# Kernel tuning notes

Hardware: AMD Instinct MI355X
Metric: run time of the kernel (lower is better)

The kernel has to match this reference:

```python
import jax, jax.numpy as jnp
import numpy as np

B, N, DIM, H, DH = 2, 1024, 1024, 8, 64
DI = H * DH  # 512
K = 4        # depthwise conv kernel
EPS = 1.1920929e-07  # float32 eps (torch RMSNorm default)


def setup_inputs() -> dict:
    key = jax.random.key(0)
    ks = jax.random.split(key, 12)
    s = lambda k, shape, sc=0.02: jax.random.normal(k, shape, jnp.float32) * sc
    return dict(
        x=jax.random.normal(ks[0], (B, N, DIM), jnp.float32),
        w_rms=jnp.ones((DIM,), jnp.float32),
        wq=s(ks[1], (DIM, DI)), wk=s(ks[2], (DIM, DI)), wv=s(ks[3], (DIM, DI)),
        wo=s(ks[4], (DI, DIM)),
        conv_q=s(ks[5], (DIM, K), 0.3), conv_k=s(ks[6], (DIM, K), 0.3), conv_v=s(ks[7], (DIM, K), 0.3),
        gamma_q=jnp.ones((H, 1, DH), jnp.float32), gamma_k=jnp.ones((H, 1, DH), jnp.float32),
        lr_w=s(ks[8], (DIM, H)), lr_b=jnp.full((H,), -4.0, jnp.float32),
        decay_w=s(ks[9], (DIM, H)), decay_b=jnp.full((H,), 4.0, jnp.float32),
        mom_w=s(ks[10], (DIM, H)), mom_b=jnp.full((H,), 2.0, jnp.float32),
    )


def rmsnorm(x, w):
    return x * jax.lax.rsqrt(jnp.mean(x * x, -1, keepdims=True) + EPS) * w


def mh_rmsnorm(x, gamma):  # x: (b, h, n, d)
    rms = jnp.sqrt(jnp.sum(x * x, -1, keepdims=True)) * (DH ** -0.5)
    return x / jnp.maximum(rms, 1e-8) * gamma


def dwconv(x, w):  # x: (b, n, dim), w: (dim, K) depthwise, padding K//2 -> length n+1
    y = jax.lax.conv_general_dilated(
        x.transpose(0, 2, 1), w[:, None, :], (1,), [(K // 2, K // 2)],
        feature_group_count=DIM, dimension_numbers=('NCW', 'OIW', 'NCW'))
    return y.transpose(0, 2, 1)


def gated_scan(a, x):  # h_t = a_t h_{t-1} + x_t, h_{-1}=0; a:(bh,t), x:(bh,t,d,d)
    def combine(c1, c2):
        a1, x1 = c1
        a2, x2 = c2
        return a1 * a2, a2 * x1 + x2
    _, h = jax.lax.associative_scan(combine, (a[..., None, None], x), axis=1)
    return h


def reference(x, w_rms, wq, wk, wv, wo, conv_q, conv_k, conv_v,
              gamma_q, gamma_k, lr_w, lr_b, decay_w, decay_b, mom_w, mom_b):
    b, n, _ = x.shape
    xa = rmsnorm(x, w_rms)
    qi, ki, vi = dwconv(xa, conv_q), dwconv(xa, conv_k), dwconv(xa, conv_v)
    split = lambda t: t.reshape(b, -1, H, DH).transpose(0, 2, 1, 3)[:, :, :n]  # (b,h,n,d)
    q = mh_rmsnorm(split(qi @ wq), gamma_q)
    k = mh_rmsnorm(split(ki @ wk), gamma_k)
    v = split(vi @ wv)
    fq = q.reshape(b * H, n, DH)
    fk = k.reshape(b * H, n, DH)
    fv = v.reshape(b * H, n, DH)
    sig = jax.nn.sigmoid
    lr = sig(xa @ lr_w + lr_b).transpose(0, 2, 1).reshape(b * H, n)
    decay = sig(xa @ decay_w + decay_b).transpose(0, 2, 1).reshape(b * H, n)
    mom = sig(xa @ mom_w + mom_b).transpose(0, 2, 1).reshape(b * H, n)
    # S_ref = S0 = 0 (fresh state) => pred = 0, delta_vec = -v
    g = jnp.einsum('bti,btj->btij', -fv, fk)          # (bh, n, d, d)
    Z = gated_scan(mom, g)                             # momentum scan
    S = gated_scan(decay, -lr[..., None, None] * Z)    # memory scan
    S_prev = jnp.concatenate([jnp.zeros_like(S[:, :1]), S[:, :-1]], axis=1)
    y = jnp.einsum('btdp,btp->btd', S_prev, fq)        # retrieval y_t = S_{t-1} psi_t
    y = y.reshape(b, H, n, DH).transpose(0, 2, 1, 3).reshape(b, n, DI)
    return y @ wo
```

## Files before the change

kernel.cpp:

```cpp
#include <hip/hip_runtime.h>
#include <math.h>

#define DEV __device__ __forceinline__

constexpr int Bb   = 2;
constexpr int Seq  = 1024;
constexpr int Dim  = 1024;
constexpr int Hh   = 8;
constexpr int Dh   = 64;
constexpr int Di   = 512;
constexpr int BN   = Bb * Seq;
constexpr int NSEQ = Bb * Hh;
constexpr int CHUNK = 32;
constexpr int CLEN  = Seq / CHUNK;
constexpr float EPSV = 1.1920929e-07f;
constexpr int NT2  = 8;
constexpr int KSPL = 8;

typedef _Float16 half8 __attribute__((ext_vector_type(8)));
typedef float    f32x4 __attribute__((ext_vector_type(4)));

DEV float bf2f(unsigned short u) {
  union { unsigned int i; float f; } x; x.i = ((unsigned int)u) << 16; return x.f;
}
DEV unsigned short f2bf(float f) {
  union { float f; unsigned int i; } x; x.f = f;
  unsigned int r = x.i + 0x7fffu + ((x.i >> 16) & 1u);
  return (unsigned short)(r >> 16);
}
DEV float ldin(const void* p, int f32, size_t i) {
  if (f32) return ((const float*)p)[i];
  return bf2f(((const unsigned short*)p)[i]);
}
DEV void ld4(const void* p, int f32, size_t i, float* dst) {
  if (f32) {
    float4 u = *(const float4*)((const float*)p + i);
    dst[0] = u.x; dst[1] = u.y; dst[2] = u.z; dst[3] = u.w;
  } else {
    ushort4 u = *(const ushort4*)((const unsigned short*)p + i);
    dst[0] = bf2f(u.x); dst[1] = bf2f(u.y); dst[2] = bf2f(u.z); dst[3] = bf2f(u.w);
  }
}
DEV int sniff_vote(const void* p, int n, int tid) {
  int j = 2 * tid, valid = 0, bad = 0;
  if (j < n) {
    valid = 1;
    float v = bf2f(((const unsigned short*)p)[j]);
    float a = fabsf(v);
    if (!(a >= 1e-12f && a <= 1e4f)) bad = 1;
  }
#pragma unroll
  for (int m = 1; m < 64; m <<= 1) { valid += __shfl_xor(valid, m); bad += __shfl_xor(bad, m); }
  return (2 * bad > valid) ? 1 : 0;
}

DEV void gld16(const _Float16* g, _Float16* l) {
  __builtin_amdgcn_global_load_lds(
      (const __attribute__((address_space(1))) void*)g,
      (__attribute__((address_space(3))) void*)l, 16, 0, 0);
}

struct InPtrs { const void* p[17]; int n[17]; };

__global__ __launch_bounds__(256) void k_prep_all(
    InPtrs ip,
    int* __restrict__ flags,
    _Float16* __restrict__ wqT, _Float16* __restrict__ wkT,
    _Float16* __restrict__ wvT, _Float16* __restrict__ woT,
    _Float16* __restrict__ WgT,
    _Float16* __restrict__ wcq, _Float16* __restrict__ wck,
    _Float16* __restrict__ wcv,
    float* __restrict__ gqf, float* __restrict__ gkf, float* __restrict__ gbf)
{
  int blk = blockIdx.x;
  int tid = threadIdx.x;
  __shared__ int sfl[8];

  if (blk < 1024) {
    int z = blk >> 8, bx = blk & 15, by = (blk >> 4) & 15;
    int idx = (z == 0) ? 2 : ((z == 1) ? 3 : ((z == 2) ? 4 : 5));
    const void* src = ip.p[idx];
    _Float16* dst   = (z == 0) ? wqT : ((z == 1) ? wkT : ((z == 2) ? wvT : woT));
    int Kd = (z < 3) ? Dim : Di;
    int Nn = (z < 3) ? Di : Dim;
    int n0 = bx * 64, k0 = by * 64;
    if (n0 >= Nn || k0 >= Kd) return;

    if (tid < 64) { int f = sniff_vote(src, ip.n[idx], tid); if (tid == 0) sfl[0] = f; }
    __syncthreads();
    int f = sfl[0];

    __shared__ float tile[64][65];
    int r = tid >> 4, c4 = (tid & 15) * 4;
#pragma unroll
    for (int rr = 0; rr < 4; ++rr) {
      int k = rr * 16 + r;
      ld4(src, f, (size_t)(k0 + k) * Nn + n0 + c4, &tile[k][c4]);
    }
    __syncthreads();
#pragma unroll
    for (int rr = 0; rr < 4; ++rr) {
      int n = rr * 16 + r;
      _Float16 o4[4];
#pragma unroll
      for (int j = 0; j < 4; ++j) o4[j] = (_Float16)tile[c4 + j][n];
      *(ushort4*)&dst[(size_t)(n0 + n) * Kd + k0 + c4] = *(ushort4*)o4;
    }
  } else if (blk < 1088) {
    int row = blk - 1024;
    if (row < 24) {
      int g = row >> 3, h = row & 7;
      int idx = (g == 0) ? 11 : ((g == 1) ? 13 : 15);
      const void* W = ip.p[idx];
      if (tid < 64) { int f = sniff_vote(W, ip.n[idx], tid); if (tid == 0) sfl[0] = f; }
      __syncthreads();
      int f = sfl[0];
#pragma unroll
      for (int it = 0; it < 4; ++it) {
        int d = it * 256 + tid;
        WgT[(size_t)row * Dim + d] = (_Float16)ldin(W, f, (size_t)d * Hh + h);
      }
    } else {
#pragma unroll
      for (int it = 0; it < 4; ++it)
        WgT[(size_t)row * Dim + it * 256 + tid] = (_Float16)0.f;
    }
  } else if (blk < 1104) {
    if (tid < 64) {
      int f6 = sniff_vote(ip.p[6], ip.n[6], tid);
      int f7 = sniff_vote(ip.p[7], ip.n[7], tid);
      int f8 = sniff_vote(ip.p[8], ip.n[8], tid);
      if (tid == 0) { sfl[0] = f6; sfl[1] = f7; sfl[2] = f8; }
    }
    __syncthreads();
    int e = (blk - 1088) * 256 + tid;
    wcq[e] = (_Float16)ldin(ip.p[6], sfl[0], e);
    wck[e] = (_Float16)ldin(ip.p[7], sfl[1], e);
    wcv[e] = (_Float16)ldin(ip.p[8], sfl[2], e);
  } else {
    __shared__ int allf[17];
    for (int ii = 0; ii < 17; ++ii) {
      if (tid < 64) {
        int f = sniff_vote(ip.p[ii], ip.n[ii], tid);
        if (tid == 0) { flags[ii] = f; allf[ii] = f; }
      }
    }
    __syncthreads();
    int f9 = allf[9], f10 = allf[10];
    for (int i = tid; i < Di; i += 256) {
      gqf[i] = ldin(ip.p[9], f9, i);
      gkf[i] = ldin(ip.p[10], f10, i);
    }
    if (tid < 24) {
      int g = tid >> 3, h = tid & 7;
      int idx = (g == 0) ? 12 : ((g == 1) ? 14 : 16);
      gbf[tid] = ldin(ip.p[idx], allf[idx], h);
    }
  }
}

__global__ __launch_bounds__(256) void k_rmsconv(
    const void* __restrict__ x, const void* __restrict__ w_rms,
    const int* __restrict__ flags,
    const _Float16* __restrict__ wcq, const _Float16* __restrict__ wck,
    const _Float16* __restrict__ wcv,
    _Float16* __restrict__ xaf,
    _Float16* __restrict__ qc, _Float16* __restrict__ kc,
    _Float16* __restrict__ vc)
{
  constexpr int NR = NT2 + 3;
  __shared__ _Float16 xas[NR][Dim];
  int tb = blockIdx.x, b = blockIdx.y;
  int t0 = tb * NT2;
  int tid = threadIdx.x, lane = tid & 63, wv = tid >> 6;
  int fx = flags[0], fw = flags[1];
  int e0 = lane * 16;

  float wr[16];
#pragma unroll
  for (int q = 0; q < 4; ++q) ld4(w_rms, fw, e0 + q * 4, &wr[q * 4]);

  for (int rr = wv; rr < NR; rr += 4) {
    int r = t0 - 2 + rr;
    float xv[16];
    bool inr = (r >= 0 && r < Seq);
    if (inr) {
      size_t rb = (size_t)(b * Seq + r) * Dim + e0;
#pragma unroll
      for (int q = 0; q < 4; ++q) ld4(x, fx, rb + q * 4, &xv[q * 4]);
    } else {
#pragma unroll
      for (int j = 0; j < 16; ++j) xv[j] = 0.f;
    }
    float ss = 0.f;
#pragma unroll
    for (int j = 0; j < 16; ++j) ss = fmaf(xv[j], xv[j], ss);
#pragma unroll
    for (int m = 1; m < 64; m <<= 1) ss += __shfl_xor(ss, m);
    float scale = rsqrtf(ss * (1.0f / Dim) + EPSV);

    _Float16 o[16];
#pragma unroll
    for (int j = 0; j < 16; ++j) o[j] = (_Float16)(xv[j] * scale * wr[j]);
    *(uint4*)&xas[rr][e0]     = *(uint4*)&o[0];
    *(uint4*)&xas[rr][e0 + 8] = *(uint4*)&o[8];
    if (inr && r >= t0 && r < t0 + NT2) {
      size_t ob = (size_t)(b * Seq + r) * Dim + e0;
      *(uint4*)&xaf[ob]     = *(uint4*)&o[0];
      *(uint4*)&xaf[ob + 8] = *(uint4*)&o[8];
    }
  }
  __syncthreads();

  int c0 = tid * 4;
  _Float16 lwq[16], lwk[16], lwv[16];
  *(uint4*)&lwq[0] = *(const uint4*)&wcq[c0 * 4];
  *(uint4*)&lwq[8] = *(const uint4*)&wcq[c0 * 4 + 8];
  *(uint4*)&lwk[0] = *(const uint4*)&wck[c0 * 4];
  *(uint4*)&lwk[8] = *(const uint4*)&wck[c0 * 4 + 8];
  *(uint4*)&lwv[0] = *(const uint4*)&wcv[c0 * 4];
  *(uint4*)&lwv[8] = *(const uint4*)&wcv[c0 * 4 + 8];

#pragma unroll
  for (int tt = 0; tt < NT2; ++tt) {
    float rv[4][4];
#pragma unroll
    for (int k = 0; k < 4; ++k) {
      _Float16 hx[4];
      *(ushort4*)hx = *(const ushort4*)&xas[tt + k][c0];
#pragma unroll
      for (int j = 0; j < 4; ++j) rv[k][j] = (float)hx[j];
    }
    _Float16 tq[4], tk[4], tv[4];
#pragma unroll
    for (int j = 0; j < 4; ++j) {
      float aq = rv[0][j] * (float)lwq[j * 4 + 0] + rv[1][j] * (float)lwq[j * 4 + 1]
               + rv[2][j] * (float)lwq[j * 4 + 2] + rv[3][j] * (float)lwq[j * 4 + 3];
      float ak = rv[0][j] * (float)lwk[j * 4 + 0] + rv[1][j] * (float)lwk[j * 4 + 1]
               + rv[2][j] * (float)lwk[j * 4 + 2] + rv[3][j] * (float)lwk[j * 4 + 3];
      float av = rv[0][j] * (float)lwv[j * 4 + 0] + rv[1][j] * (float)lwv[j * 4 + 1]
               + rv[2][j] * (float)lwv[j * 4 + 2] + rv[3][j] * (float)lwv[j * 4 + 3];
      tq[j] = (_Float16)aq; tk[j] = (_Float16)ak; tv[j] = (_Float16)av;
    }
    size_t o = ((size_t)(b * Seq + t0 + tt)) * Dim + c0;
    *(ushort4*)&qc[o] = *(ushort4*)tq;
    *(ushort4*)&kc[o] = *(ushort4*)tk;
    *(ushort4*)&vc[o] = *(ushort4*)tv;
  }
}

__global__ __launch_bounds__(256) void k_mid(
    const _Float16* __restrict__ qc, const _Float16* __restrict__ kc,
    const _Float16* __restrict__ vc,
    const _Float16* __restrict__ wqT, const _Float16* __restrict__ wkT,
    const _Float16* __restrict__ wvT,
    const _Float16* __restrict__ xaf, const _Float16* __restrict__ WgT,
    _Float16* __restrict__ qpre, _Float16* __restrict__ kpre,
    _Float16* __restrict__ vpre,
    float* __restrict__ gpart)
{
  __shared__ __align__(16) _Float16 ldsbuf[256 * 32];

  int blk = blockIdx.x;
  int tid = threadIdx.x, lane = tid & 63, wv = tid >> 6;
  int mrow = lane & 15, quad = lane >> 4;

  if (blk < 192) {
    int z = blk >> 6, rem = blk & 63;
    int by = rem >> 2, bx = rem & 3;
    const _Float16* A  = (z == 0) ? qc : ((z == 1) ? kc : vc);
    const _Float16* Bt = (z == 0) ? wqT : ((z == 1) ? wkT : wvT);
    _Float16* C        = (z == 0) ? qpre : ((z == 1) ? kpre : vpre);
    int m0 = by * 128, n0 = bx * 128;
    int wr = wv >> 1, wc = wv & 1;

    _Float16* Asl = ldsbuf;
    _Float16* Bsl = ldsbuf + 128 * 32;

    int sr = lane >> 2, sc = (lane & 3) * 8;

    f32x4 acc[4][4];
#pragma unroll
    for (int mi = 0; mi < 4; ++mi)
#pragma unroll
      for (int ni = 0; ni < 4; ++ni) acc[mi][ni] = (f32x4){0.f, 0.f, 0.f, 0.f};

    for (int kt = 0; kt < Dim; kt += 32) {
      __syncthreads();
      gld16(&A [(size_t)(m0 + wv * 32      + sr) * Dim + kt + sc], &Asl[(wv * 32     ) * 32]);
      gld16(&A [(size_t)(m0 + wv * 32 + 16 + sr) * Dim + kt + sc], &Asl[(wv * 32 + 16) * 32]);
      gld16(&Bt[(size_t)(n0 + wv * 32      + sr) * Dim + kt + sc], &Bsl[(wv * 32     ) * 32]);
      gld16(&Bt[(size_t)(n0 + wv * 32 + 16 + sr) * Dim + kt + sc], &Bsl[(wv * 32 + 16) * 32]);
      __syncthreads();

      half8 afr[4], bfr[4];
#pragma unroll
      for (int i = 0; i < 4; ++i)
        afr[i] = *(const half8*)&Asl[(wr * 64 + i * 16 + mrow) * 32 + quad * 8];
#pragma unroll
      for (int i = 0; i < 4; ++i)
        bfr[i] = *(const half8*)&Bsl[(wc * 64 + i * 16 + mrow) * 32 + quad * 8];
#pragma unroll
      for (int mi = 0; mi < 4; ++mi)
#pragma unroll
        for (int ni = 0; ni < 4; ++ni)
          acc[mi][ni] = __builtin_amdgcn_mfma_f32_16x16x32_f16(afr[mi], bfr[ni], acc[mi][ni], 0, 0, 0);
    }

#pragma unroll
    for (int mi = 0; mi < 4; ++mi) {
#pragma unroll
      for (int ni = 0; ni < 4; ++ni) {
        int col = n0 + wc * 64 + ni * 16 + mrow;
#pragma unroll
        for (int r2 = 0; r2 < 4; ++r2) {
          int row = m0 + wr * 64 + mi * 16 + quad * 4 + r2;
          C[(size_t)row * Di + col] = (_Float16)acc[mi][ni][r2];
        }
      }
    }
  } else {
    _Float16 (*As)[40] = (_Float16(*)[40])ldsbuf;
    _Float16 (*Bs)[40] = (_Float16(*)[40])(ldsbuf + 128 * 40);

    int g = blk - 192;
    int m0 = (g & 31) * 64, ks = g >> 5;
    int srow = tid >> 2, scol = (tid & 3) * 8;
    int kbase = ks * (Dim / KSPL);

    f32x4 acc[4];
#pragma unroll
    for (int mi = 0; mi < 4; ++mi) acc[mi] = (f32x4){0.f, 0.f, 0.f, 0.f};

    for (int kt = kbase; kt < kbase + Dim / KSPL; kt += 32) {
      __syncthreads();
      *(uint4*)&As[srow][scol] = *(const uint4*)&xaf[(size_t)(m0 + srow) * Dim + kt + scol];
      *(uint4*)&Bs[srow][scol] = *(const uint4*)&WgT[(size_t)srow * Dim + kt + scol];
      __syncthreads();
      half8 bfr = *(const half8*)&Bs[wv * 16 + mrow][quad * 8];
#pragma unroll
      for (int mi = 0; mi < 4; ++mi) {
        half8 afr = *(const half8*)&As[mi * 16 + mrow][quad * 8];
        acc[mi] = __builtin_amdgcn_mfma_f32_16x16x32_f16(afr, bfr, acc[mi], 0, 0, 0);
      }
    }

    int col = wv * 16 + mrow;
    if (col < 24) {
#pragma unroll
      for (int mi = 0; mi < 4; ++mi) {
#pragma unroll
        for (int r2 = 0; r2 < 4; ++r2) {
          int row = m0 + mi * 16 + quad * 4 + r2;
          gpart[((size_t)ks * BN + row) * 32 + col] = acc[mi][r2];
        }
      }
    }
  }
}

__global__ __launch_bounds__(256) void k_gemm_fin(
    const _Float16* __restrict__ A, const _Float16* __restrict__ Bt,
    void* __restrict__ C, const int* __restrict__ flags, int Nn, int Kd)
{
  __shared__ __align__(16) _Float16 lds[(128 + 64) * 32];
  _Float16* Asl = lds;
  _Float16* Bsl = lds + 128 * 32;

  int tid = threadIdx.x, lane = tid & 63, wv = tid >> 6;
  int n0 = blockIdx.x * 64, m0 = blockIdx.y * 128;
  int mrow = lane & 15, quad = lane >> 4;
  int wm = wv * 32;
  int sr = lane >> 2, sc = (lane & 3) * 8;

  f32x4 acc[2][4];
#pragma unroll
  for (int mi = 0; mi < 2; ++mi)
#pragma unroll
    for (int ni = 0; ni < 4; ++ni) acc[mi][ni] = (f32x4){0.f, 0.f, 0.f, 0.f};

  for (int kt = 0; kt < Kd; kt += 32) {
    __syncthreads();
    gld16(&A [(size_t)(m0 + wv * 32      + sr) * Kd + kt + sc], &Asl[(wv * 32     ) * 32]);
    gld16(&A [(size_t)(m0 + wv * 32 + 16 + sr) * Kd + kt + sc], &Asl[(wv * 32 + 16) * 32]);
    gld16(&Bt[(size_t)(n0 + wv * 16      + sr) * Kd + kt + sc], &Bsl[(wv * 16     ) * 32]);
    __syncthreads();

    half8 bfr[4];
#pragma unroll
    for (int ni = 0; ni < 4; ++ni)
      bfr[ni] = *(const half8*)&Bsl[(ni * 16 + mrow) * 32 + quad * 8];
#pragma unroll
    for (int mi = 0; mi < 2; ++mi) {
      half8 afr = *(const half8*)&Asl[(wm + mi * 16 + mrow) * 32 + quad * 8];
#pragma unroll
      for (int ni = 0; ni < 4; ++ni)
        acc[mi][ni] = __builtin_amdgcn_mfma_f32_16x16x32_f16(afr, bfr[ni], acc[mi][ni], 0, 0, 0);
    }
  }

  int any_bf16 = 0;
#pragma unroll
  for (int i2 = 0; i2 < 17; ++i2) any_bf16 |= (flags[i2] == 0);

#pragma unroll
  for (int mi = 0; mi < 2; ++mi) {
#pragma unroll
    for (int ni = 0; ni < 4; ++ni) {
      int col = n0 + ni * 16 + mrow;
#pragma unroll
      for (int r2 = 0; r2 < 4; ++r2) {
        int row = m0 + wm + mi * 16 + quad * 4 + r2;
        float v = acc[mi][ni][r2];
        size_t idx = (size_t)row * Nn + col;
        if (any_bf16) ((unsigned short*)C)[idx] = f2bf(v);
        else          ((float*)C)[idx] = v;
      }
    }
  }
}

DEV void load_gates(const float* __restrict__ gpart, const float* __restrict__ gbf,
                    int b, int h, int c, int tid,
                    float* gl, float* gd, float* gm)
{
  if (tid < 96) {
    int which = tid >> 5, t2 = tid & 31;
    int col = which * 8 + h;
    int row = b * Seq + c * CLEN + t2;
    float acc = gbf[col];
#pragma unroll
    for (int ks = 0; ks < KSPL; ++ks)
      acc += gpart[((size_t)ks * BN + row) * 32 + col];
    float sg = 1.f / (1.f + expf(-acc));
    if (which == 0) gl[t2] = sg; else if (which == 1) gd[t2] = sg; else gm[t2] = sg;
  }
}

__global__ __launch_bounds__(256) void k_phaseA(
    const _Float16* __restrict__ kpre, const _Float16* __restrict__ vpre,
    const float* __restrict__ gkf,
    const float* __restrict__ gpart, const float* __restrict__ gbf,
    _Float16* __restrict__ ZS_Z, _Float16* __restrict__ ZS_S,
    float* __restrict__ Mc, float* __restrict__ Dc, float* __restrict__ Wc)
{
  int c = blockIdx.x, s = blockIdx.y;
  int b = s >> 3, h = s & 7;
  int tid = threadIdx.x, lane = tid & 63, wv = tid >> 6;
  int i = tid >> 2, j0 = (tid & 3) * 16;
  __shared__ float kn[CLEN][64], vv[CLEN][64];
  __shared__ float gl[CLEN], gd[CLEN], gm[CLEN];

  {
    int t = tid >> 3, col = (tid & 7) * 8;
    size_t g = ((size_t)(b * Seq + c * CLEN + t)) * Di + h * 64 + col;
    half8 kv = *(const half8*)&kpre[g];
    half8 vvv = *(const half8*)&vpre[g];
#pragma unroll
    for (int j = 0; j < 8; ++j) { kn[t][col + j] = (float)kv[j]; vv[t][col + j] = (float)vvv[j]; }
    load_gates(gpart, gbf, b, h, c, tid, gl, gd, gm);
  }
  __syncthreads();
  {
    float gk = gkf[h * 64 + lane];
#pragma unroll
    for (int tt = 0; tt < 8; ++tt) {
      int t = wv * 8 + tt;
      float kvv = kn[t][lane];
      float ss = kvv * kvv;
#pragma unroll
      for (int m = 1; m < 64; m <<= 1) ss += __shfl_xor(ss, m);
      kn[t][lane] = kvv * (1.f / fmaxf(sqrtf(ss) * 0.125f, 1e-8f)) * gk;
    }
  }
  __syncthreads();

  float Zl[16], Sl[16];
#pragma unroll
  for (int jj = 0; jj < 16; ++jj) { Zl[jj] = 0.f; Sl[jj] = 0.f; }
  float Mcum = 1.f, Dcum = 1.f, wacc = 0.f;

  for (int t = 0; t < CLEN; ++t) {
    float l = gl[t], dd = gd[t], mm = gm[t];
    float vi = vv[t][i];
    Mcum *= mm;
#pragma unroll
    for (int jj = 0; jj < 16; ++jj) {
      Zl[jj] = fmaf(mm, Zl[jj], -vi * kn[t][j0 + jj]);
      Sl[jj] = fmaf(dd, Sl[jj], -l * Zl[jj]);
    }
    wacc = fmaf(dd, wacc, -l * Mcum);
    Dcum *= dd;
  }
  size_t base = ((size_t)(s * CHUNK + c)) * 4096 + (size_t)i * 64 + j0;
  half8 zo0, zo1, so0, so1;
#pragma unroll
  for (int jj = 0; jj < 8; ++jj) {
    zo0[jj] = (_Float16)Zl[jj];     zo1[jj] = (_Float16)Zl[jj + 8];
    so0[jj] = (_Float16)Sl[jj];     so1[jj] = (_Float16)Sl[jj + 8];
  }
  *(half8*)&ZS_Z[base] = zo0; *(half8*)&ZS_Z[base + 8] = zo1;
  *(half8*)&ZS_S[base] = so0; *(half8*)&ZS_S[base + 8] = so1;
  if (tid == 0) {
    Mc[s * CHUNK + c] = Mcum; Dc[s * CHUNK + c] = Dcum; Wc[s * CHUNK + c] = wacc;
  }
}

__global__ __launch_bounds__(256) void k_phaseB(
    _Float16* __restrict__ ZS_Z, _Float16* __restrict__ ZS_S,
    const float* __restrict__ Mc, const float* __restrict__ Dc,
    const float* __restrict__ Wc)
{
  int s = blockIdx.x;
  int e = blockIdx.y * 256 + threadIdx.x;
  float Z = 0.f, S = 0.f;
  for (int c = 0; c < CHUNK; ++c) {
    size_t base = ((size_t)(s * CHUNK + c)) * 4096 + e;
    float mc = Mc[s * CHUNK + c], dc = Dc[s * CHUNK + c], wc = Wc[s * CHUNK + c];
    float zl = (float)ZS_Z[base], sl = (float)ZS_S[base];
    ZS_Z[base] = (_Float16)Z; ZS_S[base] = (_Float16)S;
    S = fmaf(dc, S, fmaf(wc, Z, sl));
    Z = fmaf(mc, Z, zl);
  }
}

__global__ __launch_bounds__(256) void k_phaseC(
    const _Float16* __restrict__ qpre, const _Float16* __restrict__ kpre,
    const _Float16* __restrict__ vpre,
    const float* __restrict__ gqf, const float* __restrict__ gkf,
    const float* __restrict__ gpart, const float* __restrict__ gbf,
    const _Float16* __restrict__ ZS_Z, const _Float16* __restrict__ ZS_S,
    _Float16* __restrict__ yb)
{
  int c = blockIdx.x, s = blockIdx.y;
  int b = s >> 3, h = s & 7;
  int tid = threadIdx.x, lane = tid & 63, wv = tid >> 6;
  int i = tid >> 2, j0 = (tid & 3) * 16;
  __shared__ float kn[CLEN][64], vv[CLEN][64], qn[CLEN][64];
  __shared__ float gl[CLEN], gd[CLEN], gm[CLEN];

  float Zi_[16], Si_[16], Zl[16], Sl[16];
  size_t base = ((size_t)(s * CHUNK + c)) * 4096 + (size_t)i * 64 + j0;
  {
    half8 z0 = *(const half8*)&ZS_Z[base], z1 = *(const half8*)&ZS_Z[base + 8];
    half8 s0 = *(const half8*)&ZS_S[base], s1 = *(const half8*)&ZS_S[base + 8];
#pragma unroll
    for (int jj = 0; jj < 8; ++jj) {
      Zi_[jj] = (float)z0[jj]; Zi_[jj + 8] = (float)z1[jj];
      Si_[jj] = (float)s0[jj]; Si_[jj + 8] = (float)s1[jj];
      Zl[jj] = 0.f; Zl[jj + 8] = 0.f; Sl[jj] = 0.f; Sl[jj + 8] = 0.f;
    }
  }
  {
    int t = tid >> 3, col = (tid & 7) * 8;
    size_t g = ((size_t)(b * Seq + c * CLEN + t)) * Di + h * 64 + col;
    half8 kv = *(const half8*)&kpre[g];
    half8 vvv = *(const half8*)&vpre[g];
    half8 qv = *(const half8*)&qpre[g];
#pragma unroll
    for (int j = 0; j < 8; ++j) {
      kn[t][col + j] = (float)kv[j]; vv[t][col + j] = (float)vvv[j];
      qn[t][col + j] = (float)qv[j];
    }
    load_gates(gpart, gbf, b, h, c, tid, gl, gd, gm);
  }
  __syncthreads();
  {
    float gk = gkf[h * 64 + lane];
    float gq = gqf[h * 64 + lane];
#pragma unroll
    for (int tt = 0; tt < 8; ++tt) {
      int t = wv * 8 + tt;
      float kvv = kn[t][lane];
      float ssk = kvv * kvv;
      float qvv = qn[t][lane];
      float ssq = qvv * qvv;
#pragma unroll
      for (int m = 1; m < 64; m <<= 1) { ssk += __shfl_xor(ssk, m); ssq += __shfl_xor(ssq, m); }
      kn[t][lane] = kvv * (1.f / fmaxf(sqrtf(ssk) * 0.125f, 1e-8f)) * gk;
      qn[t][lane] = qvv * (1.f / fmaxf(sqrtf(ssq) * 0.125f, 1e-8f)) * gq;
    }
  }
  __syncthreads();

  float Mcum = 1.f, Dcum = 1.f, wacc = 0.f;
  float Dprev = 1.f, wprev = 0.f;

  for (int t = 0; t < CLEN; ++t) {
    float l = gl[t], dd = gd[t], mm = gm[t];

    float yp = 0.f;
#pragma unroll
    for (int jj = 0; jj < 16; ++jj) {
      float tmp = fmaf(Dprev, Si_[jj], fmaf(wprev, Zi_[jj], Sl[jj]));
      yp = fmaf(tmp, qn[t][j0 + jj], yp);
    }
    yp += __shfl_xor(yp, 1);
    yp += __shfl_xor(yp, 2);
    if ((tid & 3) == 0)
      yb[((size_t)(b * Seq + c * CLEN + t)) * Di + h * 64 + i] = (_Float16)yp;

    float vi = vv[t][i];
    Mcum *= mm;
#pragma unroll
    for (int jj = 0; jj < 16; ++jj) {
      Zl[jj] = fmaf(mm, Zl[jj], -vi * kn[t][j0 + jj]);
      Sl[jj] = fmaf(dd, Sl[jj], -l * Zl[jj]);
    }
    wacc = fmaf(dd, wacc, -l * Mcum);
    Dcum *= dd;
    Dprev = Dcum; wprev = wacc;
  }
}

extern "C" void kernel_launch(void* const* d_in, const int* in_sizes, int n_in,
                              void* d_out, int out_size, void* d_ws, size_t ws_size,
                              hipStream_t stream) {
  InPtrs ip;
  for (int i = 0; i < 17; ++i) { ip.p[i] = d_in[i]; ip.n[i] = in_sizes[i]; }

  char* p = (char*)d_ws;
  auto take = [&](size_t bytes) -> char* {
    char* q = p; p += (bytes + 255) & ~(size_t)255; return q;
  };
  int* flags           = (int*)take(32 * 4);
  _Float16* xaf        = (_Float16*)take((size_t)BN * Dim * 2);
  _Float16* qc         = (_Float16*)take((size_t)BN * Dim * 2);
  _Float16* kc         = (_Float16*)take((size_t)BN * Dim * 2);
  _Float16* vc         = (_Float16*)take((size_t)BN * Dim * 2);
  _Float16* qpre       = (_Float16*)take((size_t)BN * Di * 2);
  _Float16* kpre       = (_Float16*)take((size_t)BN * Di * 2);
  _Float16* vpre       = (_Float16*)take((size_t)BN * Di * 2);
  float* gpart         = (float*)take((size_t)KSPL * BN * 32 * 4);
  float* Mc            = (float*)take((size_t)NSEQ * CHUNK * 4);
  float* Dc            = (float*)take((size_t)NSEQ * CHUNK * 4);
  float* Wc            = (float*)take((size_t)NSEQ * CHUNK * 4);
  _Float16* wqT        = (_Float16*)take((size_t)Di * Dim * 2);
  _Float16* wkT        = (_Float16*)take((size_t)Di * Dim * 2);
  _Float16* wvT        = (_Float16*)take((size_t)Di * Dim * 2);
  _Float16* woT        = (_Float16*)take((size_t)Dim * Di * 2);
  _Float16* WgT        = (_Float16*)take((size_t)64 * Dim * 2);
  _Float16* wcq        = (_Float16*)take((size_t)Dim * 4 * 2);
  _Float16* wck        = (_Float16*)take((size_t)Dim * 4 * 2);
  _Float16* wcv        = (_Float16*)take((size_t)Dim * 4 * 2);
  float* gqf           = (float*)take(Di * 4);
  float* gkf           = (float*)take(Di * 4);
  float* gbf           = (float*)take(32 * 4);
  _Float16* ZS_Z       = qc;
  _Float16* ZS_S       = kc;
  _Float16* yb         = vc;

  k_prep_all<<<1105, 256, 0, stream>>>(ip, flags, wqT, wkT, wvT, woT, WgT,
                                       wcq, wck, wcv, gqf, gkf, gbf);

  k_rmsconv<<<dim3(Seq / NT2, Bb), 256, 0, stream>>>(
      d_in[0], d_in[1], flags, wcq, wck, wcv, xaf, qc, kc, vc);

  k_mid<<<448, 256, 0, stream>>>(qc, kc, vc, wqT, wkT, wvT, xaf, WgT,
                                 qpre, kpre, vpre, gpart);

  k_phaseA<<<dim3(CHUNK, NSEQ), 256, 0, stream>>>(kpre, vpre, gkf,
                                                  gpart, gbf,
                                                  ZS_Z, ZS_S, Mc, Dc, Wc);
  k_phaseB<<<dim3(NSEQ, 16), 256, 0, stream>>>(ZS_Z, ZS_S, Mc, Dc, Wc);
  k_phaseC<<<dim3(CHUNK, NSEQ), 256, 0, stream>>>(qpre, kpre, vpre, gqf, gkf,
                                                  gpart, gbf,
                                                  ZS_Z, ZS_S, yb);

  k_gemm_fin<<<dim3(Dim / 64, BN / 128), 256, 0, stream>>>(
      yb, woT, d_out, flags, Dim, Di);
}
```

Baseline: 184.8 us.

## Merge weight prep and rmsnorm-conv into one launch; reuse normalized k

Folds the rmsnorm+depthwise-conv kernel into the weight-prep kernel as extra blocks that read the conv weights directly from the inputs, so one kernel launch and the intermediate fp16 conv-weight buffers go away. Shared memory is unioned between the transpose tile and the conv row buffer. Phase A now writes normalized k back into kpre so phase C skips recomputing the k RMS norm. This adds extra global writes in phase A and larger per-block LDS in the merged kernel, which may lower occupancy for the transpose blocks.

```diff
diff --git a/kernel.cpp b/kernel.cpp
--- a/kernel.cpp
+++ b/kernel.cpp
@@ -62,19 +62,21 @@
 
 struct InPtrs { const void* p[17]; int n[17]; };
 
-__global__ __launch_bounds__(256) void k_prep_all(
+__global__ __launch_bounds__(256) void k_front(
     InPtrs ip,
     int* __restrict__ flags,
     _Float16* __restrict__ wqT, _Float16* __restrict__ wkT,
     _Float16* __restrict__ wvT, _Float16* __restrict__ woT,
     _Float16* __restrict__ WgT,
-    _Float16* __restrict__ wcq, _Float16* __restrict__ wck,
-    _Float16* __restrict__ wcv,
-    float* __restrict__ gqf, float* __restrict__ gkf, float* __restrict__ gbf)
+    float* __restrict__ gqf, float* __restrict__ gkf, float* __restrict__ gbf,
+    _Float16* __restrict__ xaf,
+    _Float16* __restrict__ qc, _Float16* __restrict__ kc,
+    _Float16* __restrict__ vc)
 {
   int blk = blockIdx.x;
   int tid = threadIdx.x;
   __shared__ int sfl[8];
+  __shared__ __align__(16) char smem_u[11 * Dim * 2];
 
   if (blk < 1024) {
     int z = blk >> 8, bx = blk & 15, by = (blk >> 4) & 15;
@@ -90,7 +92,7 @@
     __syncthreads();
     int f = sfl[0];
 
-    __shared__ float tile[64][65];
+    float (*tile)[65] = (float(*)[65])smem_u;
     int r = tid >> 4, c4 = (tid & 15) * 4;
 #pragma unroll
     for (int rr = 0; rr < 4; ++rr) {
@@ -125,19 +127,7 @@
       for (int it = 0; it < 4; ++it)
         WgT[(size_t)row * Dim + it * 256 + tid] = (_Float16)0.f;
     }
-  } else if (blk < 1104) {
-    if (tid < 64) {
-      int f6 = sniff_vote(ip.p[6], ip.n[6], tid);
-      int f7 = sniff_vote(ip.p[7], ip.n[7], tid);
-      int f8 = sniff_vote(ip.p[8], ip.n[8], tid);
-      if (tid == 0) { sfl[0] = f6; sfl[1] = f7; sfl[2] = f8; }
-    }
-    __syncthreads();
-    int e = (blk - 1088) * 256 + tid;
-    wcq[e] = (_Float16)ldin(ip.p[6], sfl[0], e);
-    wck[e] = (_Float16)ldin(ip.p[7], sfl[1], e);
-    wcv[e] = (_Float16)ldin(ip.p[8], sfl[2], e);
-  } else {
+  } else if (blk == 1088) {
     __shared__ int allf[17];
     for (int ii = 0; ii < 17; ++ii) {
       if (tid < 64) {
@@ -156,96 +146,98 @@
       int idx = (g == 0) ? 12 : ((g == 1) ? 14 : 16);
       gbf[tid] = ldin(ip.p[idx], allf[idx], h);
     }
-  }
-}
-
-__global__ __launch_bounds__(256) void k_rmsconv(
-    const void* __restrict__ x, const void* __restrict__ w_rms,
-    const int* __restrict__ flags,
-    const _Float16* __restrict__ wcq, const _Float16* __restrict__ wck,
-    const _Float16* __restrict__ wcv,
-    _Float16* __restrict__ xaf,
-    _Float16* __restrict__ qc, _Float16* __restrict__ kc,
-    _Float16* __restrict__ vc)
-{
-  constexpr int NR = NT2 + 3;
-  __shared__ _Float16 xas[NR][Dim];
-  int tb = blockIdx.x, b = blockIdx.y;
-  int t0 = tb * NT2;
-  int tid = threadIdx.x, lane = tid & 63, wv = tid >> 6;
-  int fx = flags[0], fw = flags[1];
-  int e0 = lane * 16;
-
-  float wr[16];
-#pragma unroll
-  for (int q = 0; q < 4; ++q) ld4(w_rms, fw, e0 + q * 4, &wr[q * 4]);
-
-  for (int rr = wv; rr < NR; rr += 4) {
-    int r = t0 - 2 + rr;
-    float xv[16];
-    bool inr = (r >= 0 && r < Seq);
-    if (inr) {
-      size_t rb = (size_t)(b * Seq + r) * Dim + e0;
-#pragma unroll
-      for (int q = 0; q < 4; ++q) ld4(x, fx, rb + q * 4, &xv[q * 4]);
-    } else {
-#pragma unroll
-      for (int j = 0; j < 16; ++j) xv[j] = 0.f;
-    }
-    float ss = 0.f;
-#pragma unroll
-    for (int j = 0; j < 16; ++j) ss = fmaf(xv[j], xv[j], ss);
-#pragma unroll
-    for (int m = 1; m < 64; m <<= 1) ss += __shfl_xor(ss, m);
-    float scale = rsqrtf(ss * (1.0f / Dim) + EPSV);
-
-    _Float16 o[16];
-#pragma unroll
-    for (int j = 0; j < 16; ++j) o[j] = (_Float16)(xv[j] * scale * wr[j]);
-    *(uint4*)&xas[rr][e0]     = *(uint4*)&o[0];
-    *(uint4*)&xas[rr][e0 + 8] = *(uint4*)&o[8];
-    if (inr && r >= t0 && r < t0 + NT2) {
-      size_t ob = (size_t)(b * Seq + r) * Dim + e0;
-      *(uint4*)&xaf[ob]     = *(uint4*)&o[0];
-      *(uint4*)&xaf[ob + 8] = *(uint4*)&o[8];
-    }
-  }
-  __syncthreads();
-
-  int c0 = tid * 4;
-  _Float16 lwq[16], lwk[16], lwv[16];
-  *(uint4*)&lwq[0] = *(const uint4*)&wcq[c0 * 4];
-  *(uint4*)&lwq[8] = *(const uint4*)&wcq[c0 * 4 + 8];
-  *(uint4*)&lwk[0] = *(const uint4*)&wck[c0 * 4];
-  *(uint4*)&lwk[8] = *(const uint4*)&wck[c0 * 4 + 8];
-  *(uint4*)&lwv[0] = *(const uint4*)&wcv[c0 * 4];
-  *(uint4*)&lwv[8] = *(const uint4*)&wcv[c0 * 4 + 8];
-
-#pragma unroll
-  for (int tt = 0; tt < NT2; ++tt) {
-    float rv[4][4];
-#pragma unroll
-    for (int k = 0; k < 4; ++k) {
-      _Float16 hx[4];
-      *(ushort4*)hx = *(const ushort4*)&xas[tt + k][c0];
-#pragma unroll
-      for (int j = 0; j < 4; ++j) rv[k][j] = (float)hx[j];
-    }
-    _Float16 tq[4], tk[4], tv[4];
-#pragma unroll
-    for (int j = 0; j < 4; ++j) {
-      float aq = rv[0][j] * (float)lwq[j * 4 + 0] + rv[1][j] * (float)lwq[j * 4 + 1]
-               + rv[2][j] * (float)lwq[j * 4 + 2] + rv[3][j] * (float)lwq[j * 4 + 3];
-      float ak = rv[0][j] * (float)lwk[j * 4 + 0] + rv[1][j] * (float)lwk[j * 4 + 1]
-               + rv[2][j] * (float)lwk[j * 4 + 2] + rv[3][j] * (float)lwk[j * 4 + 3];
-      float av = rv[0][j] * (float)lwv[j * 4 + 0] + rv[1][j] * (float)lwv[j * 4 + 1]
-               + rv[2][j] * (float)lwv[j * 4 + 2] + rv[3][j] * (float)lwv[j * 4 + 3];
-      tq[j] = (_Float16)aq; tk[j] = (_Float16)ak; tv[j] = (_Float16)av;
-    }
-    size_t o = ((size_t)(b * Seq + t0 + tt)) * Dim + c0;
-    *(ushort4*)&qc[o] = *(ushort4*)tq;
-    *(ushort4*)&kc[o] = *(ushort4*)tk;
-    *(ushort4*)&vc[o] = *(ushort4*)tv;
+  } else {
+    constexpr int NR = NT2 + 3;
+    _Float16 (*xas)[Dim] = (_Float16(*)[Dim])smem_u;
+
+    int rb = blk - 1089;
+    int tb = rb & 127, b = rb >> 7;
+    int t0 = tb * NT2;
+    int lane = tid & 63, wv = tid >> 6;
+
+    if (tid < 64) {
+      int f0 = sniff_vote(ip.p[0], ip.n[0], tid);
+      int f1 = sniff_vote(ip.p[1], ip.n[1], tid);
+      int f6 = sniff_vote(ip.p[6], ip.n[6], tid);
+      int f7 = sniff_vote(ip.p[7], ip.n[7], tid);
+      int f8 = sniff_vote(ip.p[8], ip.n[8], tid);
+      if (tid == 0) { sfl[0] = f0; sfl[1] = f1; sfl[2] = f6; sfl[3] = f7; sfl[4] = f8; }
+    }
+    __syncthreads();
+    int fx = sfl[0], fw = sfl[1], f6 = sfl[2], f7 = sfl[3], f8 = sfl[4];
+    int e0 = lane * 16;
+
+    float wr[16];
+#pragma unroll
+    for (int q = 0; q < 4; ++q) ld4(ip.p[1], fw, e0 + q * 4, &wr[q * 4]);
+
+    for (int rr = wv; rr < NR; rr += 4) {
+      int r = t0 - 2 + rr;
+      float xv[16];
+      bool inr = (r >= 0 && r < Seq);
+      if (inr) {
+        size_t rbx = (size_t)(b * Seq + r) * Dim + e0;
+#pragma unroll
+        for (int q = 0; q < 4; ++q) ld4(ip.p[0], fx, rbx + q * 4, &xv[q * 4]);
+      } else {
+#pragma unroll
+        for (int j = 0; j < 16; ++j) xv[j] = 0.f;
+      }
+      float ss = 0.f;
+#pragma unroll
+      for (int j = 0; j < 16; ++j) ss = fmaf(xv[j], xv[j], ss);
+#pragma unroll
+      for (int m = 1; m < 64; m <<= 1) ss += __shfl_xor(ss, m);
+      float scale = rsqrtf(ss * (1.0f / Dim) + EPSV);
+
+      _Float16 o[16];
+#pragma unroll
+      for (int j = 0; j < 16; ++j) o[j] = (_Float16)(xv[j] * scale * wr[j]);
+      *(uint4*)&xas[rr][e0]     = *(uint4*)&o[0];
+      *(uint4*)&xas[rr][e0 + 8] = *(uint4*)&o[8];
+      if (inr && r >= t0 && r < t0 + NT2) {
+        size_t ob = (size_t)(b * Seq + r) * Dim + e0;
+        *(uint4*)&xaf[ob]     = *(uint4*)&o[0];
+        *(uint4*)&xaf[ob + 8] = *(uint4*)&o[8];
+      }
+    }
+    __syncthreads();
+
+    int c0 = tid * 4;
+    float lwq[16], lwk[16], lwv[16];
+#pragma unroll
+    for (int q = 0; q < 4; ++q) {
+      ld4(ip.p[6], f6, (size_t)c0 * 4 + q * 4, &lwq[q * 4]);
+      ld4(ip.p[7], f7, (size_t)c0 * 4 + q * 4, &lwk[q * 4]);
+      ld4(ip.p[8], f8, (size_t)c0 * 4 + q * 4, &lwv[q * 4]);
+    }
+
+#pragma unroll
+    for (int tt = 0; tt < NT2; ++tt) {
+      float rv[4][4];
+#pragma unroll
+      for (int k = 0; k < 4; ++k) {
+        _Float16 hx[4];
+        *(ushort4*)hx = *(const ushort4*)&xas[tt + k][c0];
+#pragma unroll
+        for (int j = 0; j < 4; ++j) rv[k][j] = (float)hx[j];
+      }
+      _Float16 tq[4], tk[4], tv[4];
+#pragma unroll
+      for (int j = 0; j < 4; ++j) {
+        float aq = rv[0][j] * lwq[j * 4 + 0] + rv[1][j] * lwq[j * 4 + 1]
+                 + rv[2][j] * lwq[j * 4 + 2] + rv[3][j] * lwq[j * 4 + 3];
+        float ak = rv[0][j] * lwk[j * 4 + 0] + rv[1][j] * lwk[j * 4 + 1]
+                 + rv[2][j] * lwk[j * 4 + 2] + rv[3][j] * lwk[j * 4 + 3];
+        float av = rv[0][j] * lwv[j * 4 + 0] + rv[1][j] * lwv[j * 4 + 1]
+                 + rv[2][j] * lwv[j * 4 + 2] + rv[3][j] * lwv[j * 4 + 3];
+        tq[j] = (_Float16)aq; tk[j] = (_Float16)ak; tv[j] = (_Float16)av;
+      }
+      size_t o = ((size_t)(b * Seq + t0 + tt)) * Dim + c0;
+      *(ushort4*)&qc[o] = *(ushort4*)tq;
+      *(ushort4*)&kc[o] = *(ushort4*)tk;
+      *(ushort4*)&vc[o] = *(ushort4*)tv;
+    }
   }
 }
 
@@ -438,7 +430,7 @@
 }
 
 __global__ __launch_bounds__(256) void k_phaseA(
-    const _Float16* __restrict__ kpre, const _Float16* __restrict__ vpre,
+    _Float16* __restrict__ kpre, const _Float16* __restrict__ vpre,
     const float* __restrict__ gkf,
     const float* __restrict__ gpart, const float* __restrict__ gbf,
     _Float16* __restrict__ ZS_Z, _Float16* __restrict__ ZS_S,
@@ -470,7 +462,9 @@
       float ss = kvv * kvv;
 #pragma unroll
       for (int m = 1; m < 64; m <<= 1) ss += __shfl_xor(ss, m);
-      kn[t][lane] = kvv * (1.f / fmaxf(sqrtf(ss) * 0.125f, 1e-8f)) * gk;
+      float knv = kvv * (1.f / fmaxf(sqrtf(ss) * 0.125f, 1e-8f)) * gk;
+      kn[t][lane] = knv;
+      kpre[((size_t)(b * Seq + c * CLEN + t)) * Di + h * 64 + lane] = (_Float16)knv;
     }
   }
   __syncthreads();
@@ -527,7 +521,7 @@
 __global__ __launch_bounds__(256) void k_phaseC(
     const _Float16* __restrict__ qpre, const _Float16* __restrict__ kpre,
     const _Float16* __restrict__ vpre,
-    const float* __restrict__ gqf, const float* __restrict__ gkf,
+    const float* __restrict__ gqf,
     const float* __restrict__ gpart, const float* __restrict__ gbf,
     const _Float16* __restrict__ ZS_Z, const _Float16* __restrict__ ZS_S,
     _Float16* __restrict__ yb)
@@ -566,18 +560,14 @@
   }
   __syncthreads();
   {
-    float gk = gkf[h * 64 + lane];
     float gq = gqf[h * 64 + lane];
 #pragma unroll
     for (int tt = 0; tt < 8; ++tt) {
       int t = wv * 8 + tt;
-      float kvv = kn[t][lane];
-      float ssk = kvv * kvv;
       float qvv = qn[t][lane];
       float ssq = qvv * qvv;
 #pragma unroll
-      for (int m = 1; m < 64; m <<= 1) { ssk += __shfl_xor(ssk, m); ssq += __shfl_xor(ssq, m); }
-      kn[t][lane] = kvv * (1.f / fmaxf(sqrtf(ssk) * 0.125f, 1e-8f)) * gk;
+      for (int m = 1; m < 64; m <<= 1) ssq += __shfl_xor(ssq, m);
       qn[t][lane] = qvv * (1.f / fmaxf(sqrtf(ssq) * 0.125f, 1e-8f)) * gq;
     }
   }
@@ -640,9 +630,6 @@
   _Float16* wvT        = (_Float16*)take((size_t)Di * Dim * 2);
   _Float16* woT        = (_Float16*)take((size_t)Dim * Di * 2);
   _Float16* WgT        = (_Float16*)take((size_t)64 * Dim * 2);
-  _Float16* wcq        = (_Float16*)take((size_t)Dim * 4 * 2);
-  _Float16* wck        = (_Float16*)take((size_t)Dim * 4 * 2);
-  _Float16* wcv        = (_Float16*)take((size_t)Dim * 4 * 2);
   float* gqf           = (float*)take(Di * 4);
   float* gkf           = (float*)take(Di * 4);
   float* gbf           = (float*)take(32 * 4);
@@ -650,11 +637,8 @@
   _Float16* ZS_S       = kc;
   _Float16* yb         = vc;
 
-  k_prep_all<<<1105, 256, 0, stream>>>(ip, flags, wqT, wkT, wvT, woT, WgT,
-                                       wcq, wck, wcv, gqf, gkf, gbf);
-
-  k_rmsconv<<<dim3(Seq / NT2, Bb), 256, 0, stream>>>(
-      d_in[0], d_in[1], flags, wcq, wck, wcv, xaf, qc, kc, vc);
+  k_front<<<1345, 256, 0, stream>>>(ip, flags, wqT, wkT, wvT, woT, WgT,
+                                    gqf, gkf, gbf, xaf, qc, kc, vc);
 
   k_mid<<<448, 256, 0, stream>>>(qc, kc, vc, wqT, wkT, wvT, xaf, WgT,
                                  qpre, kpre, vpre, gpart);
@@ -663,7 +647,7 @@
                                                   gpart, gbf,
                                                   ZS_Z, ZS_S, Mc, Dc, Wc);
   k_phaseB<<<dim3(NSEQ, 16), 256, 0, stream>>>(ZS_Z, ZS_S, Mc, Dc, Wc);
-  k_phaseC<<<dim3(CHUNK, NSEQ), 256, 0, stream>>>(qpre, kpre, vpre, gqf, gkf,
+  k_phaseC<<<dim3(CHUNK, NSEQ), 256, 0, stream>>>(qpre, kpre, vpre, gqf,
                                                   gpart, gbf,
                                                   ZS_Z, ZS_S, yb);
 
```

Result: faster. 181.0 us (-2.1%).
